# Optimization experiments

Hardware: AMD Instinct MI355X
Metric: run time of the kernel (lower is better)

Reference implementation:

```python
import jax, jax.numpy as jnp
import numpy as np

D_K = 128

def setup_inputs() -> dict:
    key = jax.random.key(0)
    k1, k2, k3 = jax.random.split(key, 3)
    q = jax.random.normal(k1, (8192, D_K), dtype=jnp.float32)
    k = jax.random.normal(k2, (8192, D_K), dtype=jnp.float32)
    v = jax.random.normal(k3, (8192, D_K), dtype=jnp.float32)
    return {"q": q, "k": k, "v": v}

def reference(q, k, v):
    # scores: [S_q, S_k]
    scores = jnp.einsum('qd,kd->qk', q, k) / jnp.sqrt(jnp.float32(D_K))
    attn = jax.nn.softmax(scores, axis=-1)  # softmax over keys (torch default last dim)
    return jnp.einsum('qk,kd->qd', attn, v)
```

## Files before the change

### kernel.cpp

```cpp
#include <hip/hip_runtime.h>
#include <math.h>


typedef _Float16 f16x8 __attribute__((ext_vector_type(8)));
typedef float    f32x16 __attribute__((ext_vector_type(16)));

constexpr int S_LEN = 8192;
constexpr int D_K   = 128;
constexpr int NSLICE = 8;
constexpr int ITERS2 = (S_LEN / NSLICE) / 64;

constexpr size_t WS_L_OFF = 0;
constexpr size_t KV_OFF   = 262144;
constexpr size_t PART_OFF = KV_OFF + (size_t)256 * 16384;
constexpr size_t WS_NEED  = PART_OFF + (size_t)7 * S_LEN * D_K * 4;

#define CSCALE (0.08838834764831845f * 1.44269504088896340736f)

union UH8 { _Float16 h[8]; uint4 q; f16x8 v; };
union UF4 { unsigned u[4]; uint4 q; f16x8 v; };

__device__ inline void async16(const uint4* g, uint4* l) {
  __builtin_amdgcn_global_load_lds(
      (const __attribute__((address_space(1))) unsigned int*)g,
      (__attribute__((address_space(3))) unsigned int*)l, 16, 0, 0);
}

template <bool ZOUT>
__global__ __launch_bounds__(512) void attn_prep(const float* __restrict__ K,
                                                 const float* __restrict__ V,
                                                 float* __restrict__ out,
                                                 char* __restrict__ ws) {
  const int t = blockIdx.x * 512 + threadIdx.x;
  uint4* KVg = (uint4*)(ws + KV_OFF);
  if (t < 131072) {
    int kt = t >> 9, idx = t & 511;
    int lane = idx & 63, s = idx >> 6;
    int key = kt * 32 + (lane & 31);
    int d0  = s * 16 + (lane >> 5) * 8;
    const float4* src = (const float4*)(K + (size_t)key * D_K + d0);
    float4 a = src[0], b = src[1];
    float f[8] = {a.x, a.y, a.z, a.w, b.x, b.y, b.z, b.w};
    UH8 h;
    #pragma unroll
    for (int j = 0; j < 8; ++j) h.h[j] = (_Float16)f[j];
    KVg[(size_t)kt * 1024 + idx] = h.q;
  } else if (t < 262144) {
    int g = t - 131072;
    int kt = g >> 9, idx = g & 511;
    int lane = idx & 63, c = (idx >> 6) & 3, kstep = idx >> 8;
    int d  = c * 32 + (lane & 31);
    int kb = kt * 32 + kstep * 16 + (lane >> 5) * 8;
    UH8 h;
    #pragma unroll
    for (int j = 0; j < 8; ++j) h.h[j] = (_Float16)V[(size_t)(kb + j) * D_K + d];
    KVg[(size_t)kt * 1024 + 512 + idx] = h.q;
  } else if (ZOUT && t < 327680) {
    int i = t - 262144;
    float4 z = make_float4(0.f, 0.f, 0.f, 0.f);
    float4* o4 = (float4*)out;
    #pragma unroll
    for (int j = 0; j < 4; ++j) o4[(size_t)i * 4 + j] = z;
  } else if (ZOUT && t < 329728) {
    int i = t - 327680;
    ((float4*)(ws + WS_L_OFF))[i] = make_float4(0.f, 0.f, 0.f, 0.f);
  }
}

__device__ inline void qk32(const uint4* sub, const f16x8* qf, int lane,
                            f32x16& Sa, f32x16& Sb) {
  Sa = f32x16{}; Sb = f32x16{};
  __builtin_amdgcn_s_setprio(1);
  #pragma unroll
  for (int s = 0; s < 4; ++s) {
    f16x8 ka = __builtin_bit_cast(f16x8, sub[(2 * s    ) * 64 + lane]);
    f16x8 kb = __builtin_bit_cast(f16x8, sub[(2 * s + 1) * 64 + lane]);
    Sa = __builtin_amdgcn_mfma_f32_32x32x16_f16(ka, qf[2 * s    ], Sa, 0, 0, 0);
    Sb = __builtin_amdgcn_mfma_f32_32x32x16_f16(kb, qf[2 * s + 1], Sb, 0, 0, 0);
  }
  __builtin_amdgcn_s_setprio(0);
}

__device__ inline void softmax32(const f32x16& Sa, const f32x16& Sb,
                                 float& lsum, UF4& A0, UF4& A1) {
  unsigned pk[8];
  #pragma unroll
  for (int i = 0; i < 8; ++i) {
    float p0 = __builtin_amdgcn_exp2f(Sa[2 * i]     + Sb[2 * i]);
    float p1 = __builtin_amdgcn_exp2f(Sa[2 * i + 1] + Sb[2 * i + 1]);
    lsum += p0 + p1;
    pk[i] = __builtin_bit_cast(unsigned, __builtin_amdgcn_cvt_pkrtz(p0, p1));
  }
  auto r0 = __builtin_amdgcn_permlane32_swap((int)pk[0], (int)pk[2], false, false);
  auto r1 = __builtin_amdgcn_permlane32_swap((int)pk[1], (int)pk[3], false, false);
  auto r2 = __builtin_amdgcn_permlane32_swap((int)pk[4], (int)pk[6], false, false);
  auto r3 = __builtin_amdgcn_permlane32_swap((int)pk[5], (int)pk[7], false, false);
  A0.u[0] = (unsigned)r0[0]; A0.u[2] = (unsigned)r0[1];
  A0.u[1] = (unsigned)r1[0]; A0.u[3] = (unsigned)r1[1];
  A1.u[0] = (unsigned)r2[0]; A1.u[2] = (unsigned)r2[1];
  A1.u[1] = (unsigned)r3[0]; A1.u[3] = (unsigned)r3[1];
}

__device__ inline void pv32(const uint4* sub, const UF4& A0, const UF4& A1,
                            int lane, f32x16* O) {
  __builtin_amdgcn_s_setprio(1);
  #pragma unroll
  for (int kstep = 0; kstep < 2; ++kstep) {
    f16x8 pf = kstep ? A1.v : A0.v;
    f16x8 v0 = __builtin_bit_cast(f16x8, sub[512 + kstep * 256 +   0 + lane]);
    f16x8 v1 = __builtin_bit_cast(f16x8, sub[512 + kstep * 256 +  64 + lane]);
    f16x8 v2 = __builtin_bit_cast(f16x8, sub[512 + kstep * 256 + 128 + lane]);
    f16x8 v3 = __builtin_bit_cast(f16x8, sub[512 + kstep * 256 + 192 + lane]);
    O[0] = __builtin_amdgcn_mfma_f32_32x32x16_f16(pf, v0, O[0], 0, 0, 0);
    O[1] = __builtin_amdgcn_mfma_f32_32x32x16_f16(pf, v1, O[1], 0, 0, 0);
    O[2] = __builtin_amdgcn_mfma_f32_32x32x16_f16(pf, v2, O[2], 0, 0, 0);
    O[3] = __builtin_amdgcn_mfma_f32_32x32x16_f16(pf, v3, O[3], 0, 0, 0);
  }
  __builtin_amdgcn_s_setprio(0);
}

template <bool PARTIAL>
__global__ __launch_bounds__(512, 2)
void attn_main(const float* __restrict__ Qg, float* __restrict__ out,
               char* __restrict__ ws) {
  __shared__ uint4 KV[3][2048];

  const int tid   = threadIdx.x;
  const int wave  = tid >> 6;
  const int lane  = tid & 63;
  const int lrow  = lane & 31;
  const int lhalf = lane >> 5;
  const int g1    = wave >> 2;

  const int blk = blockIdx.x;
  const int ks  = blk & 7;
  const int qb  = blk >> 3;
  const int qw  = qb * 256 + wave * 32;

  float* ws_l = (float*)(ws + WS_L_OFF);

  f16x8 qf[8];
  {
    const int q = qw + lrow;
    #pragma unroll
    for (int s = 0; s < 8; ++s) {
      const float4* src = (const float4*)(Qg + (size_t)q * D_K + s * 16 + lhalf * 8);
      float4 a = src[0], b = src[1];
      float f[8] = {a.x, a.y, a.z, a.w, b.x, b.y, b.z, b.w};
      UH8 h;
      #pragma unroll
      for (int j = 0; j < 8; ++j) h.h[j] = (_Float16)(f[j] * CSCALE);
      qf[s] = h.v;
    }
  }

  f32x16 O[4] = {f32x16{}, f32x16{}, f32x16{}, f32x16{}};
  float lsum = 0.f;

  const uint4* KVg = (const uint4*)(ws + KV_OFF);

  {
    const size_t base = (size_t)ks * 32768;
    #pragma unroll
    for (int i = 0; i < 4; ++i)
      async16(KVg + base + i * 512 + tid, &KV[0][i * 512 + tid]);
  }

  UF4 A1c0, A1c1;
  const uint4* sub1prev = &KV[0][1024];

  int cur = 0, nxt = 1;
  for (int it = 0; it < ITERS2; ++it) {
    __syncthreads();

    if (it + 1 < ITERS2) {
      const size_t base = (size_t)ks * 32768 + (size_t)(it + 1) * 2048;
      #pragma unroll
      for (int i = 0; i < 4; ++i)
        async16(KVg + base + i * 512 + tid, &KV[nxt][i * 512 + tid]);
    }

    const uint4* sub0 = &KV[cur][0];
    const uint4* sub1 = &KV[cur][1024];

    if (!g1) {
      f32x16 Sa, Sb;
      UF4 A0, A1;
      qk32(sub0, qf, lane, Sa, Sb);
      softmax32(Sa, Sb, lsum, A0, A1);
      pv32(sub0, A0, A1, lane, O);
      qk32(sub1, qf, lane, Sa, Sb);
      softmax32(Sa, Sb, lsum, A0, A1);
      pv32(sub1, A0, A1, lane, O);
    } else {
      if (it) pv32(sub1prev, A1c0, A1c1, lane, O);
      f32x16 Sa, Sb;
      UF4 A0, A1;
      qk32(sub0, qf, lane, Sa, Sb);
      softmax32(Sa, Sb, lsum, A0, A1);
      pv32(sub0, A0, A1, lane, O);
      qk32(sub1, qf, lane, Sa, Sb);
      softmax32(Sa, Sb, lsum, A1c0, A1c1);
      sub1prev = sub1;
    }

    cur = nxt;
    nxt = (nxt == 2) ? 0 : nxt + 1;
  }
  if (g1) pv32(sub1prev, A1c0, A1c1, lane, O);

  lsum += __shfl_xor(lsum, 32);

  if (PARTIAL) {
    if (lhalf == 0) ws_l[ks * S_LEN + qw + lrow] = lsum;
    float* obase = (ks == 0) ? out
                 : (float*)(ws + PART_OFF) + (size_t)(ks - 1) * S_LEN * D_K;
    #pragma unroll
    for (int r = 0; r < 16; ++r) {
      int row = (r & 3) + 8 * (r >> 2) + 4 * lhalf;
      float* dst = obase + (size_t)(qw + row) * D_K + lrow;
      dst[ 0] = O[0][r];
      dst[32] = O[1][r];
      dst[64] = O[2][r];
      dst[96] = O[3][r];
    }
  } else {
    if (lhalf == 0) atomicAdd(ws_l + qw + lrow, lsum);
    #pragma unroll
    for (int r = 0; r < 16; ++r) {
      int row = (r & 3) + 8 * (r >> 2) + 4 * lhalf;
      float* dst = out + (size_t)(qw + row) * D_K + lrow;
      atomicAdd(dst +  0, O[0][r]);
      atomicAdd(dst + 32, O[1][r]);
      atomicAdd(dst + 64, O[2][r]);
      atomicAdd(dst + 96, O[3][r]);
    }
  }
}

__global__ __launch_bounds__(256) void attn_norm(float* __restrict__ out,
                                                 const float* __restrict__ lpart,
                                                 const float* __restrict__ opart,
                                                 int nparts) {
  int i = blockIdx.x * 256 + threadIdx.x;
  int q = i >> 5;
  float4* o4 = (float4*)out;
  float4 acc = o4[i];
  float l = lpart[q];
  for (int s = 1; s <= nparts; ++s) {
    float4 p = ((const float4*)opart)[(size_t)(s - 1) * 262144 + i];
    acc.x += p.x; acc.y += p.y; acc.z += p.z; acc.w += p.w;
    l += lpart[s * S_LEN + q];
  }
  float inv = 1.0f / l;
  acc.x *= inv; acc.y *= inv; acc.z *= inv; acc.w *= inv;
  o4[i] = acc;
}

extern "C" void kernel_launch(void* const* d_in, const int* in_sizes, int n_in,
                              void* d_out, int out_size, void* d_ws, size_t ws_size,
                              hipStream_t stream) {
  const float* q = (const float*)d_in[0];
  const float* k = (const float*)d_in[1];
  const float* v = (const float*)d_in[2];
  float* out = (float*)d_out;
  char* ws = (char*)d_ws;

  if (ws_size >= WS_NEED) {
    attn_prep<false><<<dim3(512), dim3(512), 0, stream>>>(k, v, out, ws);
    attn_main<true><<<dim3(256), dim3(512), 0, stream>>>(q, out, ws);
    attn_norm<<<dim3(1024), dim3(256), 0, stream>>>(
        out, (const float*)(ws + WS_L_OFF), (const float*)(ws + PART_OFF), 7);
  } else {
    attn_prep<true><<<dim3(645), dim3(512), 0, stream>>>(k, v, out, ws);
    attn_main<false><<<dim3(256), dim3(512), 0, stream>>>(q, out, ws);
    attn_norm<<<dim3(1024), dim3(256), 0, stream>>>(
        out, (const float*)(ws + WS_L_OFF), (const float*)(ws + PART_OFF), 0);
  }
}
```

Baseline: 110.3 us.

## Software-pipeline attention loop: issue QK for current tile, PV for previous tile

Replaces the asymmetric two-group wave schedule with a uniform software pipeline. Every wave computes QK scores for both sub-tiles of the current KV buffer, then runs PV on the previous iteration's probabilities, then does the softmax for the current scores. The intent is to overlap MFMA work with the exp/softmax VALU work in all waves. This holds more live registers (four score accumulators plus four cached probability fragments) and relies on the triple-buffered LDS keeping the previous tile valid.

```diff
diff --git a/kernel.cpp b/kernel.cpp
--- a/kernel.cpp
+++ b/kernel.cpp
@@ -130,7 +130,6 @@
   const int lane  = tid & 63;
   const int lrow  = lane & 31;
   const int lhalf = lane >> 5;
-  const int g1    = wave >> 2;
 
   const int blk = blockIdx.x;
   const int ks  = blk & 7;
@@ -158,56 +157,46 @@
   float lsum = 0.f;
 
   const uint4* KVg = (const uint4*)(ws + KV_OFF);
-
-  {
-    const size_t base = (size_t)ks * 32768;
-    #pragma unroll
-    for (int i = 0; i < 4; ++i)
-      async16(KVg + base + i * 512 + tid, &KV[0][i * 512 + tid]);
-  }
-
-  UF4 A1c0, A1c1;
-  const uint4* sub1prev = &KV[0][1024];
+  const size_t sbase = (size_t)ks * 32768;
+
+  #pragma unroll
+  for (int i = 0; i < 4; ++i)
+    async16(KVg + sbase + i * 512 + tid, &KV[0][i * 512 + tid]);
+
+  UF4 C00, C01, C10, C11;
 
   int cur = 0, nxt = 1;
   for (int it = 0; it < ITERS2; ++it) {
     __syncthreads();
 
     if (it + 1 < ITERS2) {
-      const size_t base = (size_t)ks * 32768 + (size_t)(it + 1) * 2048;
+      const size_t base = sbase + (size_t)(it + 1) * 2048;
       #pragma unroll
       for (int i = 0; i < 4; ++i)
         async16(KVg + base + i * 512 + tid, &KV[nxt][i * 512 + tid]);
     }
 
-    const uint4* sub0 = &KV[cur][0];
-    const uint4* sub1 = &KV[cur][1024];
-
-    if (!g1) {
-      f32x16 Sa, Sb;
-      UF4 A0, A1;
-      qk32(sub0, qf, lane, Sa, Sb);
-      softmax32(Sa, Sb, lsum, A0, A1);
-      pv32(sub0, A0, A1, lane, O);
-      qk32(sub1, qf, lane, Sa, Sb);
-      softmax32(Sa, Sb, lsum, A0, A1);
-      pv32(sub1, A0, A1, lane, O);
-    } else {
-      if (it) pv32(sub1prev, A1c0, A1c1, lane, O);
-      f32x16 Sa, Sb;
-      UF4 A0, A1;
-      qk32(sub0, qf, lane, Sa, Sb);
-      softmax32(Sa, Sb, lsum, A0, A1);
-      pv32(sub0, A0, A1, lane, O);
-      qk32(sub1, qf, lane, Sa, Sb);
-      softmax32(Sa, Sb, lsum, A1c0, A1c1);
-      sub1prev = sub1;
-    }
+    f32x16 Sa0, Sb0, Sa1, Sb1;
+    qk32(&KV[cur][0],    qf, lane, Sa0, Sb0);
+    qk32(&KV[cur][1024], qf, lane, Sa1, Sb1);
+
+    if (it) {
+      const int prv = (cur == 0) ? 2 : cur - 1;
+      pv32(&KV[prv][0],    C00, C01, lane, O);
+      pv32(&KV[prv][1024], C10, C11, lane, O);
+    }
+
+    softmax32(Sa0, Sb0, lsum, C00, C01);
+    softmax32(Sa1, Sb1, lsum, C10, C11);
 
     cur = nxt;
     nxt = (nxt == 2) ? 0 : nxt + 1;
   }
-  if (g1) pv32(sub1prev, A1c0, A1c1, lane, O);
+  {
+    const int prv = (cur == 0) ? 2 : cur - 1;
+    pv32(&KV[prv][0],    C00, C01, lane, O);
+    pv32(&KV[prv][1024], C10, C11, lane, O);
+  }
 
   lsum += __shfl_xor(lsum, 32);
 
```

New measurement: 109.8 us. About the same (-0.4%).
